# Kernel optimization log

Measured on AMD Instinct MI355X. Metric: run time of the kernel, lower is better.

## Reference

```python
import jax, jax.numpy as jnp
import numpy as np

N = 50000          # nodes
E = 800000         # edges (avg degree 16)
IN, HID, OUT = 128, 128, 32
BN_EPS = 1e-5


def gcn_conv(x, W, b, src, dst):
    """PyG GCNConv: D^-1/2 (A+I) D^-1/2 (x @ W) + b, self-loops included."""
    h = x @ W                                                  # [N, out]
    ones = jnp.ones((src.shape[0],), dtype=x.dtype)
    deg = jax.ops.segment_sum(ones, dst, num_segments=N) + 1.0  # in-degree + self-loop
    dis = jax.lax.rsqrt(deg)                                    # deg^-1/2
    norm = dis[src] * dis[dst]                                  # [E]
    msg = h[src] * norm[:, None]                                # gather + scale, [E, out]
    agg = jax.ops.segment_sum(msg, dst, num_segments=N)         # scatter-add
    agg = agg + h * (dis * dis)[:, None]                        # self-loop term (norm = 1/deg_i)
    return agg + b


def bn_relu(h, g, be):
    # BatchNorm1d in training mode: batch statistics over the node dimension
    mu = jnp.mean(h, axis=0)
    var = jnp.mean((h - mu) ** 2, axis=0)  # biased variance, as torch BN
    return jax.nn.relu((h - mu) * jax.lax.rsqrt(var + BN_EPS) * g + be)


def setup_inputs() -> dict:
    key = jax.random.key(0)
    ks = jax.random.split(key, 8)
    x = jax.random.normal(ks[0], (N, IN), dtype=jnp.float32)
    edge_index = jax.random.randint(ks[1], (2, E), 0, N, dtype=jnp.int64)
    W0 = jax.random.normal(ks[2], (IN, HID), dtype=jnp.float32) / np.sqrt(IN)
    W1 = jax.random.normal(ks[3], (HID, HID), dtype=jnp.float32) / np.sqrt(HID)
    W2 = jax.random.normal(ks[4], (HID, OUT), dtype=jnp.float32) / np.sqrt(HID)
    return {
        "x": x, "edge_index": edge_index,
        "W0": W0, "b0": jnp.zeros((HID,), jnp.float32),
        "g0": jnp.ones((HID,), jnp.float32), "be0": jnp.zeros((HID,), jnp.float32),
        "W1": W1, "b1": jnp.zeros((HID,), jnp.float32),
        "g1": jnp.ones((HID,), jnp.float32), "be1": jnp.zeros((HID,), jnp.float32),
        "W2": W2, "b2": jnp.zeros((OUT,), jnp.float32),
    }


def reference(x, edge_index, W0, b0, g0, be0, W1, b1, g1, be1, W2, b2):
    src, dst = edge_index[0], edge_index[1]
    # block 0: conv -> BN -> ReLU -> (dropout: eval, identity) -> residual
    h = bn_relu(gcn_conv(x, W0, b0, src, dst), g0, be0)
    x = h + x  # use_residual, in_channels == hidden, res_proj is None
    # block 1
    h = bn_relu(gcn_conv(x, W1, b1, src, dst), g1, be1)
    x = h + x
    # final conv + log_softmax over classes
    out = gcn_conv(x, W2, b2, src, dst)
    return jax.nn.log_softmax(out, axis=1)
```

## Files before the change

### kernel.cpp

```cpp
#include <hip/hip_runtime.h>
#include <math.h>

#define NN 50000
#define NNP (NN + 1)
#define NE 800000
#define NEP 1150000
#define NBLK 49
#define NBKT 7
#define BCAP 262144

typedef __attribute__((ext_vector_type(8))) short short8;
typedef __attribute__((ext_vector_type(4))) float float4v;

__device__ inline unsigned int f2bf(float f) {
  unsigned int u = __float_as_uint(f);
  return (u + 0x7fffu + ((u >> 16) & 1u)) >> 16;
}
__device__ inline unsigned int pack2bf(float lo, float hi) {
  return f2bf(lo) | (f2bf(hi) << 16);
}
__device__ inline float bflo(unsigned int p) { return __uint_as_float(p << 16); }
__device__ inline float bfhi(unsigned int p) { return __uint_as_float(p & 0xffff0000u); }

__device__ inline void bn_fold(const float* __restrict__ gstat, const float* __restrict__ g,
                               const float* __restrict__ be, float* __restrict__ bnabS, int tid) {
  if (tid < 128) {
    float s = 0.f, q = 0.f;
    #pragma unroll
    for (int r = 0; r < 8; r++) {
      s += gstat[r * 256 + tid];
      q += gstat[r * 256 + 128 + tid];
    }
    const float inv = 1.f / (float)NN;
    float m = s * inv;
    float var = q * inv - m * m;
    float a = rsqrtf(var + 1e-5f) * g[tid];
    bnabS[tid] = a;
    bnabS[128 + tid] = be[tid] - m * a;
  }
}


__global__ __launch_bounds__(256) void k_init(int* __restrict__ deg8, float* __restrict__ gstat,
                                              int* __restrict__ csr, int* __restrict__ binCnt,
                                              const float* __restrict__ W0, const float* __restrict__ W1,
                                              const float* __restrict__ W2,
                                              unsigned short* __restrict__ wt16) {
  int i = blockIdx.x * 256 + threadIdx.x;
  if (i < NEP) csr[i] = NN;
  if (i < 8 * NN) deg8[i] = 0;
  if (i < 4096) gstat[i] = 0.f;
  if (i < NBKT) binCnt[i] = 0;
  if (i < 32768) {
    int w = i >> 14;
    int rem = i & 16383;
    int k = rem >> 7;
    int n = rem & 127;
    const float* W = w ? W1 : W0;
    wt16[w * 16384 + n * 128 + k] = (unsigned short)f2bf(W[k * 128 + n]);
  } else if (i < 36864) {
    int idx = i - 32768;
    int n = idx >> 7;
    int k = idx & 127;
    wt16[32768 + n * 128 + k] = (unsigned short)f2bf(W2[k * 32 + n]);
  }
}


__global__ __launch_bounds__(1024) void k_binA(const int* __restrict__ src, const int* __restrict__ dst,
                                               int* __restrict__ deg8, int* __restrict__ binCnt,
                                               int2* __restrict__ bin) {
  __shared__ int lcnt[NBKT], lbase[NBKT];
  int tid = threadIdx.x;
  if (tid < NBKT) lcnt[tid] = 0;
  __syncthreads();
  int e = blockIdx.x * 1024 + tid;
  bool act = e < NE;
  int d = 0, s = 0, b = 0, rank = 0;
  if (act) {
    d = dst[e]; s = src[e];
    b = d >> 13;
    atomicAdd(&deg8[(e & 7) * NN + d], 1);
    rank = atomicAdd(&lcnt[b], 1);
  }
  __syncthreads();
  if (tid < NBKT && lcnt[tid] > 0) lbase[tid] = atomicAdd(&binCnt[tid], lcnt[tid]);
  __syncthreads();
  if (act) bin[(size_t)b * BCAP + lbase[b] + rank] = make_int2(d, s);
}

__global__ __launch_bounds__(1024) void k_scan1(const int* __restrict__ deg8, int* __restrict__ degtot,
                                                int* __restrict__ excl, int* __restrict__ blksum) {
  __shared__ int sm[1024];
  int t = threadIdx.x;
  int i = blockIdx.x * 1024 + t;
  int tot = 0;
  if (i < NN) {
    #pragma unroll
    for (int j = 0; j < 8; j++) tot += deg8[j * NN + i];
    degtot[i] = tot;
  }
  int v = (i < NN) ? ((tot + 7) & ~7) : 0;
  sm[t] = v;
  __syncthreads();
  for (int off = 1; off < 1024; off <<= 1) {
    int x = (t >= off) ? sm[t - off] : 0;
    __syncthreads();
    sm[t] += x;
    __syncthreads();
  }
  if (i < NN) excl[i] = sm[t] - v;
  if (t == 1023) blksum[blockIdx.x] = sm[t];
}

__global__ void k_scan2(const int* __restrict__ blksum, int* __restrict__ blkoff,
                        int* __restrict__ rowstart) {
  int t = threadIdx.x;
  int orig = (t < NBLK) ? blksum[t] : 0;
  int v = orig;
  #pragma unroll
  for (int off = 1; off < 64; off <<= 1) {
    int u = __shfl_up(v, off);
    if (t >= off) v += u;
  }
  if (t < NBLK) blkoff[t] = v - orig;
  if (t == NBLK - 1) rowstart[NN] = v;
}

__global__ __launch_bounds__(256) void k_scan3(int* __restrict__ excl, const int* __restrict__ blkoff,
                                               const int* __restrict__ degtot, int* __restrict__ cursor,
                                               float* __restrict__ dis,
                                               unsigned short* __restrict__ hs16, float* __restrict__ h2) {
  int i = blockIdx.x * 256 + threadIdx.x;
  if (i < NN) {
    int rs = excl[i] + blkoff[i >> 10];
    excl[i] = rs;
    cursor[i] = rs;
    dis[i] = rsqrtf((float)degtot[i] + 1.0f);
  }
  if (i < 64) {
    int slice = i >> 5, c = i & 31;
    ((unsigned int*)(hs16 + (size_t)slice * ((size_t)NNP * 64) + (size_t)NN * 64))[c] = 0u;
  }
  if (i < 32) h2[(size_t)NN * 32 + i] = 0.f;
}


__global__ __launch_bounds__(256) void k_fillB(const int2* __restrict__ bin, const int* __restrict__ binCnt,
                                               int* __restrict__ cursor, int* __restrict__ csr_src) {
  int b = blockIdx.x & 7;
  if (b >= NBKT) return;
  int q = blockIdx.x >> 3;
  int cnt = binCnt[b];
  const int2* __restrict__ B = bin + (size_t)b * BCAP;
  for (int i = q * 256 + threadIdx.x; i < cnt; i += 64 * 256) {
    int2 ds = B[i];
    int p = atomicAdd(&cursor[ds.x], 1);
    csr_src[p] = ds.y;
  }
}


__global__ __launch_bounds__(256) void k_gemm128(const float* __restrict__ X,
                                                 const unsigned short* __restrict__ Wt,
                                                 const float* __restrict__ dis,
                                                 unsigned short* __restrict__ hs16, int M) {
  __shared__ char smem[52224];
  unsigned short* A  = (unsigned short*)smem;
  unsigned short* Bt = (unsigned short*)(smem + 17408);
  float* C = (float*)smem;
  const int tid = threadIdx.x;
  const int row0 = blockIdx.x * 64;

  {
    int c4 = tid & 31;
    #pragma unroll
    for (int i = 0; i < 8; i++) {
      int r = (tid >> 5) + i * 8;
      int gr = row0 + r;
      float4 v = make_float4(0.f, 0.f, 0.f, 0.f);
      if (gr < M) v = *(const float4*)(X + (size_t)gr * 128 + c4 * 4);
      *(uint2*)(A + r * 136 + c4 * 4) = make_uint2(pack2bf(v.x, v.y), pack2bf(v.z, v.w));
    }
  }
  {
    int r = tid >> 1, h = (tid & 1) * 64;
    const uint4* src = (const uint4*)(Wt + r * 128 + h);
    uint4* dst = (uint4*)(Bt + r * 136 + h);
    #pragma unroll
    for (int i = 0; i < 8; i++) dst[i] = src[i];
  }
  __syncthreads();

  const int wv = tid >> 6;
  const int l = tid & 63;
  const int lm = l & 15;
  const int lq = l >> 4;

  float4v acc[8];
  #pragma unroll
  for (int j = 0; j < 8; j++) acc[j] = (float4v)(0.f);

  const unsigned short* Arow = A + (wv * 16 + lm) * 136 + lq * 8;
  #pragma unroll
  for (int ks = 0; ks < 4; ks++) {
    short8 af = *(const short8*)(Arow + ks * 32);
    #pragma unroll
    for (int j = 0; j < 8; j++) {
      short8 bf = *(const short8*)(Bt + (j * 16 + lm) * 136 + lq * 8 + ks * 32);
      acc[j] = __builtin_amdgcn_mfma_f32_16x16x32_bf16(af, bf, acc[j], 0, 0, 0);
    }
  }
  __syncthreads();

  #pragma unroll
  for (int j = 0; j < 8; j++) {
    int col = j * 16 + lm;
    int rbase = wv * 16 + lq * 4;
    #pragma unroll
    for (int r = 0; r < 4; r++) C[(rbase + r) * 132 + col] = acc[j][r];
  }
  __syncthreads();

  {
    #pragma unroll
    for (int i = 0; i < 4; i++) {
      int idx = tid + i * 256;
      int slice = idx >> 9;
      int r = (idx >> 3) & 63;
      int ch = idx & 7;
      int gr = row0 + r;
      if (gr < M) {
        float d = dis[gr];
        const float* cp = C + r * 132 + slice * 64 + ch * 8;
        uint4 u;
        u.x = pack2bf(cp[0] * d, cp[1] * d);
        u.y = pack2bf(cp[2] * d, cp[3] * d);
        u.z = pack2bf(cp[4] * d, cp[5] * d);
        u.w = pack2bf(cp[6] * d, cp[7] * d);
        *(uint4*)(hs16 + (size_t)slice * ((size_t)NNP * 64) + (size_t)gr * 64 + ch * 8) = u;
      }
    }
  }
}


__global__ __launch_bounds__(256) void k_gemm128f(const unsigned short* __restrict__ O16,
                                                  const float* __restrict__ Xin,
                                                  unsigned short* __restrict__ XA16,
                                                  const float* __restrict__ gstat,
                                                  const float* __restrict__ g,
                                                  const float* __restrict__ be,
                                                  const unsigned short* __restrict__ Wt,
                                                  const float* __restrict__ dis,
                                                  unsigned short* __restrict__ hs16, int M) {
  __shared__ char smem[52224];
  __shared__ float bnabS[256];
  unsigned short* A  = (unsigned short*)smem;
  unsigned short* Bt = (unsigned short*)(smem + 17408);
  float* C = (float*)smem;
  const int tid = threadIdx.x;
  const int row0 = blockIdx.x * 64;

  bn_fold(gstat, g, be, bnabS, tid);
  __syncthreads();

  {
    int c = tid & 15;
    float4 alo = *(const float4*)(bnabS + c * 8);
    float4 ahi = *(const float4*)(bnabS + c * 8 + 4);
    float4 clo = *(const float4*)(bnabS + 128 + c * 8);
    float4 chi = *(const float4*)(bnabS + 128 + c * 8 + 4);
    #pragma unroll
    for (int i = 0; i < 4; i++) {
      int r = (tid >> 4) + i * 16;
      int gr = row0 + r;
      uint4 u = make_uint4(0u, 0u, 0u, 0u);
      if (gr < M) {
        uint4 ou = *(const uint4*)(O16 + (size_t)gr * 128 + c * 8);
        float4 xlo = *(const float4*)(Xin + (size_t)gr * 128 + c * 8);
        float4 xhi = *(const float4*)(Xin + (size_t)gr * 128 + c * 8 + 4);
        float v0 = fmaxf(bflo(ou.x) * alo.x + clo.x, 0.f) + xlo.x;
        float v1 = fmaxf(bfhi(ou.x) * alo.y + clo.y, 0.f) + xlo.y;
        float v2 = fmaxf(bflo(ou.y) * alo.z + clo.z, 0.f) + xlo.z;
        float v3 = fmaxf(bfhi(ou.y) * alo.w + clo.w, 0.f) + xlo.w;
        float v4 = fmaxf(bflo(ou.z) * ahi.x + chi.x, 0.f) + xhi.x;
        float v5 = fmaxf(bfhi(ou.z) * ahi.y + chi.y, 0.f) + xhi.y;
        float v6 = fmaxf(bflo(ou.w) * ahi.z + chi.z, 0.f) + xhi.z;
        float v7 = fmaxf(bfhi(ou.w) * ahi.w + chi.w, 0.f) + xhi.w;
        u.x = pack2bf(v0, v1);
        u.y = pack2bf(v2, v3);
        u.z = pack2bf(v4, v5);
        u.w = pack2bf(v6, v7);
        *(uint4*)(XA16 + (size_t)gr * 128 + c * 8) = u;
      }
      *(uint4*)(A + r * 136 + c * 8) = u;
    }
  }
  {
    int r = tid >> 1, h = (tid & 1) * 64;
    const uint4* src = (const uint4*)(Wt + r * 128 + h);
    uint4* dst = (uint4*)(Bt + r * 136 + h);
    #pragma unroll
    for (int i = 0; i < 8; i++) dst[i] = src[i];
  }
  __syncthreads();

  const int wv = tid >> 6;
  const int l = tid & 63;
  const int lm = l & 15;
  const int lq = l >> 4;

  float4v acc[8];
  #pragma unroll
  for (int j = 0; j < 8; j++) acc[j] = (float4v)(0.f);

  const unsigned short* Arow = A + (wv * 16 + lm) * 136 + lq * 8;
  #pragma unroll
  for (int ks = 0; ks < 4; ks++) {
    short8 af = *(const short8*)(Arow + ks * 32);
    #pragma unroll
    for (int j = 0; j < 8; j++) {
      short8 bf = *(const short8*)(Bt + (j * 16 + lm) * 136 + lq * 8 + ks * 32);
      acc[j] = __builtin_amdgcn_mfma_f32_16x16x32_bf16(af, bf, acc[j], 0, 0, 0);
    }
  }
  __syncthreads();

  #pragma unroll
  for (int j = 0; j < 8; j++) {
    int col = j * 16 + lm;
    int rbase = wv * 16 + lq * 4;
    #pragma unroll
    for (int r = 0; r < 4; r++) C[(rbase + r) * 132 + col] = acc[j][r];
  }
  __syncthreads();

  {
    #pragma unroll
    for (int i = 0; i < 4; i++) {
      int idx = tid + i * 256;
      int slice = idx >> 9;
      int r = (idx >> 3) & 63;
      int ch = idx & 7;
      int gr = row0 + r;
      if (gr < M) {
        float d = dis[gr];
        const float* cp = C + r * 132 + slice * 64 + ch * 8;
        uint4 u;
        u.x = pack2bf(cp[0] * d, cp[1] * d);
        u.y = pack2bf(cp[2] * d, cp[3] * d);
        u.z = pack2bf(cp[4] * d, cp[5] * d);
        u.w = pack2bf(cp[6] * d, cp[7] * d);
        *(uint4*)(hs16 + (size_t)slice * ((size_t)NNP * 64) + (size_t)gr * 64 + ch * 8) = u;
      }
    }
  }
}


__global__ __launch_bounds__(256) void k_gemm32mf(const unsigned short* __restrict__ O16,
                                                  const unsigned short* __restrict__ XA16,
                                                  const float* __restrict__ gstat,
                                                  const float* __restrict__ g,
                                                  const float* __restrict__ be,
                                                  const unsigned short* __restrict__ Wt2,
                                                  const float* __restrict__ dis,
                                                  float* __restrict__ H, int M) {
  __shared__ char smem[26112];
  __shared__ float bnabS[256];
  unsigned short* A   = (unsigned short*)smem;
  unsigned short* Bt2 = (unsigned short*)(smem + 17408);
  float* C = (float*)smem;
  const int tid = threadIdx.x;
  const int row0 = blockIdx.x * 64;

  bn_fold(gstat, g, be, bnabS, tid);
  __syncthreads();

  {
    int c = tid & 15;
    float4 alo = *(const float4*)(bnabS + c * 8);
    float4 ahi = *(const float4*)(bnabS + c * 8 + 4);
    float4 clo = *(const float4*)(bnabS + 128 + c * 8);
    float4 chi = *(const float4*)(bnabS + 128 + c * 8 + 4);
    #pragma unroll
    for (int i = 0; i < 4; i++) {
      int r = (tid >> 4) + i * 16;
      int gr = row0 + r;
      uint4 u = make_uint4(0u, 0u, 0u, 0u);
      if (gr < M) {
        uint4 ou = *(const uint4*)(O16 + (size_t)gr * 128 + c * 8);
        uint4 xu = *(const uint4*)(XA16 + (size_t)gr * 128 + c * 8);
        float v0 = fmaxf(bflo(ou.x) * alo.x + clo.x, 0.f) + bflo(xu.x);
        float v1 = fmaxf(bfhi(ou.x) * alo.y + clo.y, 0.f) + bfhi(xu.x);
        float v2 = fmaxf(bflo(ou.y) * alo.z + clo.z, 0.f) + bflo(xu.y);
        float v3 = fmaxf(bfhi(ou.y) * alo.w + clo.w, 0.f) + bfhi(xu.y);
        float v4 = fmaxf(bflo(ou.z) * ahi.x + chi.x, 0.f) + bflo(xu.z);
        float v5 = fmaxf(bfhi(ou.z) * ahi.y + chi.y, 0.f) + bfhi(xu.z);
        float v6 = fmaxf(bflo(ou.w) * ahi.z + chi.z, 0.f) + bflo(xu.w);
        float v7 = fmaxf(bfhi(ou.w) * ahi.w + chi.w, 0.f) + bfhi(xu.w);
        u.x = pack2bf(v0, v1);
        u.y = pack2bf(v2, v3);
        u.z = pack2bf(v4, v5);
        u.w = pack2bf(v6, v7);
      }
      *(uint4*)(A + r * 136 + c * 8) = u;
    }
  }
  {
    int r = tid >> 3, h = (tid & 7) * 16;
    const uint4* src = (const uint4*)(Wt2 + r * 128 + h);
    uint4* dst = (uint4*)(Bt2 + r * 136 + h);
    dst[0] = src[0];
    dst[1] = src[1];
  }
  __syncthreads();

  const int wv = tid >> 6;
  const int l = tid & 63;
  const int lm = l & 15;
  const int lq = l >> 4;

  float4v acc[2];
  acc[0] = (float4v)(0.f);
  acc[1] = (float4v)(0.f);

  const unsigned short* Arow = A + (wv * 16 + lm) * 136 + lq * 8;
  #pragma unroll
  for (int ks = 0; ks < 4; ks++) {
    short8 af = *(const short8*)(Arow + ks * 32);
    #pragma unroll
    for (int j = 0; j < 2; j++) {
      short8 bf = *(const short8*)(Bt2 + (j * 16 + lm) * 136 + lq * 8 + ks * 32);
      acc[j] = __builtin_amdgcn_mfma_f32_16x16x32_bf16(af, bf, acc[j], 0, 0, 0);
    }
  }
  __syncthreads();

  #pragma unroll
  for (int j = 0; j < 2; j++) {
    int col = j * 16 + lm;
    int rbase = wv * 16 + lq * 4;
    #pragma unroll
    for (int r = 0; r < 4; r++) C[(rbase + r) * 36 + col] = acc[j][r];
  }
  __syncthreads();

  {
    #pragma unroll
    for (int i = 0; i < 2; i++) {
      int idx = tid + i * 256;
      int r = idx >> 3;
      int ch = idx & 7;
      int gr = row0 + r;
      if (gr < M) {
        float d = dis[gr];
        const float* cp = C + r * 36 + ch * 4;
        float4 v = make_float4(cp[0] * d, cp[1] * d, cp[2] * d, cp[3] * d);
        *(float4*)(H + (size_t)gr * 32 + ch * 4) = v;
      }
    }
  }
}


__global__ __launch_bounds__(256) void k_agg128s(const unsigned short* __restrict__ Hs,
                                                 const float* __restrict__ dis,
                                                 const int* __restrict__ rowstart,
                                                 const int* __restrict__ csr_src,
                                                 const float* __restrict__ bias,
                                                 unsigned short* __restrict__ out16,
                                                 float* __restrict__ gstat) {
  __shared__ float smS[4][128], smQ[4][128];
  const int tid = threadIdx.x;
  const int wv = tid >> 6;
  const int lane = tid & 63;
  const int node_sub = lane >> 3;
  const int fl = lane & 7;
  const int base = node_sub * 8;
  const int w = blockIdx.x * 32 + wv * 8 + node_sub;
  const bool act = w < NN;
  const unsigned short* __restrict__ S0 = Hs + fl * 8;
  const unsigned short* __restrict__ S1 = Hs + (size_t)NNP * 64 + fl * 8;
  float di = act ? dis[w] : 0.f;
  int e0 = 0, e1 = 0;
  if (act) { e0 = rowstart[w]; e1 = rowstart[w + 1]; }

  float a0[8], a1[8];
  #pragma unroll
  for (int j = 0; j < 8; j++) { a0[j] = 0.f; a1[j] = 0.f; }

  int idxCur = (e0 < e1) ? csr_src[e0 + fl] : 0;
  for (int e = e0; e < e1; e += 8) {
    int cur = idxCur;
    if (e + 8 < e1) idxCur = csr_src[e + 8 + fl];
    int s0 = __shfl(cur, base + 0), s1 = __shfl(cur, base + 1);
    int s2 = __shfl(cur, base + 2), s3 = __shfl(cur, base + 3);
    int s4 = __shfl(cur, base + 4), s5 = __shfl(cur, base + 5);
    int s6 = __shfl(cur, base + 6), s7 = __shfl(cur, base + 7);
    uint4 g0 = *(const uint4*)(S0 + (size_t)s0 * 64);
    uint4 g1 = *(const uint4*)(S0 + (size_t)s1 * 64);
    uint4 g2 = *(const uint4*)(S0 + (size_t)s2 * 64);
    uint4 g3 = *(const uint4*)(S0 + (size_t)s3 * 64);
    uint4 g4 = *(const uint4*)(S0 + (size_t)s4 * 64);
    uint4 g5 = *(const uint4*)(S0 + (size_t)s5 * 64);
    uint4 g6 = *(const uint4*)(S0 + (size_t)s6 * 64);
    uint4 g7 = *(const uint4*)(S0 + (size_t)s7 * 64);
    uint4 h0 = *(const uint4*)(S1 + (size_t)s0 * 64);
    uint4 h1 = *(const uint4*)(S1 + (size_t)s1 * 64);
    uint4 h2 = *(const uint4*)(S1 + (size_t)s2 * 64);
    uint4 h3 = *(const uint4*)(S1 + (size_t)s3 * 64);
    uint4 h4 = *(const uint4*)(S1 + (size_t)s4 * 64);
    uint4 h5 = *(const uint4*)(S1 + (size_t)s5 * 64);
    uint4 h6 = *(const uint4*)(S1 + (size_t)s6 * 64);
    uint4 h7 = *(const uint4*)(S1 + (size_t)s7 * 64);
    a0[0] += ((bflo(g0.x) + bflo(g1.x)) + (bflo(g2.x) + bflo(g3.x))) + ((bflo(g4.x) + bflo(g5.x)) + (bflo(g6.x) + bflo(g7.x)));
    a0[1] += ((bfhi(g0.x) + bfhi(g1.x)) + (bfhi(g2.x) + bfhi(g3.x))) + ((bfhi(g4.x) + bfhi(g5.x)) + (bfhi(g6.x) + bfhi(g7.x)));
    a0[2] += ((bflo(g0.y) + bflo(g1.y)) + (bflo(g2.y) + bflo(g3.y))) + ((bflo(g4.y) + bflo(g5.y)) + (bflo(g6.y) + bflo(g7.y)));
    a0[3] += ((bfhi(g0.y) + bfhi(g1.y)) + (bfhi(g2.y) + bfhi(g3.y))) + ((bfhi(g4.y) + bfhi(g5.y)) + (bfhi(g6.y) + bfhi(g7.y)));
    a0[4] += ((bflo(g0.z) + bflo(g1.z)) + (bflo(g2.z) + bflo(g3.z))) + ((bflo(g4.z) + bflo(g5.z)) + (bflo(g6.z) + bflo(g7.z)));
    a0[5] += ((bfhi(g0.z) + bfhi(g1.z)) + (bfhi(g2.z) + bfhi(g3.z))) + ((bfhi(g4.z) + bfhi(g5.z)) + (bfhi(g6.z) + bfhi(g7.z)));
    a0[6] += ((bflo(g0.w) + bflo(g1.w)) + (bflo(g2.w) + bflo(g3.w))) + ((bflo(g4.w) + bflo(g5.w)) + (bflo(g6.w) + bflo(g7.w)));
    a0[7] += ((bfhi(g0.w) + bfhi(g1.w)) + (bfhi(g2.w) + bfhi(g3.w))) + ((bfhi(g4.w) + bfhi(g5.w)) + (bfhi(g6.w) + bfhi(g7.w)));
    a1[0] += ((bflo(h0.x) + bflo(h1.x)) + (bflo(h2.x) + bflo(h3.x))) + ((bflo(h4.x) + bflo(h5.x)) + (bflo(h6.x) + bflo(h7.x)));
    a1[1] += ((bfhi(h0.x) + bfhi(h1.x)) + (bfhi(h2.x) + bfhi(h3.x))) + ((bfhi(h4.x) + bfhi(h5.x)) + (bfhi(h6.x) + bfhi(h7.x)));
    a1[2] += ((bflo(h0.y) + bflo(h1.y)) + (bflo(h2.y) + bflo(h3.y))) + ((bflo(h4.y) + bflo(h5.y)) + (bflo(h6.y) + bflo(h7.y)));
    a1[3] += ((bfhi(h0.y) + bfhi(h1.y)) + (bfhi(h2.y) + bfhi(h3.y))) + ((bfhi(h4.y) + bfhi(h5.y)) + (bfhi(h6.y) + bfhi(h7.y)));
    a1[4] += ((bflo(h0.z) + bflo(h1.z)) + (bflo(h2.z) + bflo(h3.z))) + ((bflo(h4.z) + bflo(h5.z)) + (bflo(h6.z) + bflo(h7.z)));
    a1[5] += ((bfhi(h0.z) + bfhi(h1.z)) + (bfhi(h2.z) + bfhi(h3.z))) + ((bfhi(h4.z) + bfhi(h5.z)) + (bfhi(h6.z) + bfhi(h7.z)));
    a1[6] += ((bflo(h0.w) + bflo(h1.w)) + (bflo(h2.w) + bflo(h3.w))) + ((bflo(h4.w) + bflo(h5.w)) + (bflo(h6.w) + bflo(h7.w)));
    a1[7] += ((bfhi(h0.w) + bfhi(h1.w)) + (bfhi(h2.w) + bfhi(h3.w))) + ((bfhi(h4.w) + bfhi(h5.w)) + (bfhi(h6.w) + bfhi(h7.w)));
  }

  float rv0[8], rv1[8];
  if (act) {
    uint4 sv0 = *(const uint4*)(S0 + (size_t)w * 64);
    uint4 sv1 = *(const uint4*)(S1 + (size_t)w * 64);
    float se0[8] = { bflo(sv0.x), bfhi(sv0.x), bflo(sv0.y), bfhi(sv0.y),
                     bflo(sv0.z), bfhi(sv0.z), bflo(sv0.w), bfhi(sv0.w) };
    float se1[8] = { bflo(sv1.x), bfhi(sv1.x), bflo(sv1.y), bfhi(sv1.y),
                     bflo(sv1.z), bfhi(sv1.z), bflo(sv1.w), bfhi(sv1.w) };
    #pragma unroll
    for (int j = 0; j < 8; j++) {
      rv0[j] = (a0[j] + se0[j]) * di + bias[fl * 8 + j];
      rv1[j] = (a1[j] + se1[j]) * di + bias[64 + fl * 8 + j];
    }
    uint4 u0, u1;
    u0.x = pack2bf(rv0[0], rv0[1]); u0.y = pack2bf(rv0[2], rv0[3]);
    u0.z = pack2bf(rv0[4], rv0[5]); u0.w = pack2bf(rv0[6], rv0[7]);
    u1.x = pack2bf(rv1[0], rv1[1]); u1.y = pack2bf(rv1[2], rv1[3]);
    u1.z = pack2bf(rv1[4], rv1[5]); u1.w = pack2bf(rv1[6], rv1[7]);
    *(uint4*)(out16 + (size_t)w * 128 + fl * 8)      = u0;
    *(uint4*)(out16 + (size_t)w * 128 + 64 + fl * 8) = u1;
  } else {
    #pragma unroll
    for (int j = 0; j < 8; j++) { rv0[j] = 0.f; rv1[j] = 0.f; }
  }

  float q0[8], q1[8];
  #pragma unroll
  for (int j = 0; j < 8; j++) { q0[j] = rv0[j] * rv0[j]; q1[j] = rv1[j] * rv1[j]; }
  #pragma unroll
  for (int off = 8; off <= 32; off <<= 1) {
    #pragma unroll
    for (int j = 0; j < 8; j++) {
      rv0[j] += __shfl_xor(rv0[j], off);
      q0[j]  += __shfl_xor(q0[j], off);
      rv1[j] += __shfl_xor(rv1[j], off);
      q1[j]  += __shfl_xor(q1[j], off);
    }
  }
  if (node_sub == 0) {
    #pragma unroll
    for (int j = 0; j < 8; j++) {
      smS[wv][fl * 8 + j] = rv0[j];      smQ[wv][fl * 8 + j] = q0[j];
      smS[wv][64 + fl * 8 + j] = rv1[j]; smQ[wv][64 + fl * 8 + j] = q1[j];
    }
  }
  __syncthreads();
  if (tid < 128) {
    float s = (smS[0][tid] + smS[1][tid]) + (smS[2][tid] + smS[3][tid]);
    float q = (smQ[0][tid] + smQ[1][tid]) + (smQ[2][tid] + smQ[3][tid]);
    int rep = blockIdx.x & 7;
    atomicAdd(&gstat[rep * 256 + tid], s);
    atomicAdd(&gstat[rep * 256 + 128 + tid], q);
  }
}


__global__ __launch_bounds__(256) void k_agg32lsm(const float* __restrict__ H2,
                                                  const float* __restrict__ dis,
                                                  const int* __restrict__ rowstart,
                                                  const int* __restrict__ csr_src,
                                                  const float* __restrict__ bias,
                                                  float* __restrict__ out) {
  int wave = (blockIdx.x * 256 + threadIdx.x) >> 6;
  int lane = threadIdx.x & 63;
  int half = lane >> 5;
  int l = lane & 31;
  int hbase = half * 32;
  int w = wave * 2 + half;
  if (w >= NN) return;
  const float* __restrict__ S = H2 + l;
  float di = dis[w];
  int e0 = rowstart[w], e1 = rowstart[w + 1];
  float acc = 0.f;
  for (int e = e0; e < e1; e += 8) {
    int myIdx = csr_src[e + (l & 7)];
    int s0 = __shfl(myIdx, hbase + 0), s1 = __shfl(myIdx, hbase + 1);
    int s2 = __shfl(myIdx, hbase + 2), s3 = __shfl(myIdx, hbase + 3);
    int s4 = __shfl(myIdx, hbase + 4), s5 = __shfl(myIdx, hbase + 5);
    int s6 = __shfl(myIdx, hbase + 6), s7 = __shfl(myIdx, hbase + 7);
    float h0 = S[(size_t)s0 * 32], h1 = S[(size_t)s1 * 32];
    float h2v = S[(size_t)s2 * 32], h3 = S[(size_t)s3 * 32];
    float h4 = S[(size_t)s4 * 32], h5 = S[(size_t)s5 * 32];
    float h6 = S[(size_t)s6 * 32], h7 = S[(size_t)s7 * 32];
    acc += ((h0 + h1) + (h2v + h3)) + ((h4 + h5) + (h6 + h7));
  }
  float v = (acc + S[(size_t)w * 32]) * di + bias[l];
  float m = v;
  #pragma unroll
  for (int off = 16; off >= 1; off >>= 1) m = fmaxf(m, __shfl_xor(m, off));
  float ex = expf(v - m);
  float s = ex;
  #pragma unroll
  for (int off = 16; off >= 1; off >>= 1) s += __shfl_xor(s, off);
  out[(size_t)w * 32 + l] = v - m - logf(s);
}


extern "C" void kernel_launch(void* const* d_in, const int* in_sizes, int n_in,
                              void* d_out, int out_size, void* d_ws, size_t ws_size,
                              hipStream_t stream) {
  const float* x   = (const float*)d_in[0];
  const int*   ei  = (const int*)d_in[1];
  const float* W0  = (const float*)d_in[2];
  const float* b0  = (const float*)d_in[3];
  const float* g0  = (const float*)d_in[4];
  const float* be0 = (const float*)d_in[5];
  const float* W1  = (const float*)d_in[6];
  const float* b1  = (const float*)d_in[7];
  const float* g1  = (const float*)d_in[8];
  const float* be1 = (const float*)d_in[9];
  const float* W2  = (const float*)d_in[10];
  const float* b2  = (const float*)d_in[11];
  float* out = (float*)d_out;
  const int* srcI = ei;
  const int* dstI = ei + NE;

  char* p = (char*)d_ws;
  auto take = [&](size_t bytes) { char* r = p; p += (bytes + 255) & ~(size_t)255; return (void*)r; };
  int*   deg8     = (int*)take((size_t)8 * NN * 4);
  int*   cursor   = (int*)take(NN * 4);
  int*   degtot   = (int*)take(NN * 4);
  int*   rowstart = (int*)take((NN + 1) * 4);
  int*   blksum   = (int*)take(64 * 4);
  int*   blkoff   = (int*)take(64 * 4);
  int*   binCnt   = (int*)take(8 * 4);
  float* dis      = (float*)take(NN * 4);
  int*   csr      = (int*)take((size_t)NEP * 4);
  int2*  bin      = (int2*)take((size_t)NBKT * BCAP * 8);
  float* gstat    = (float*)take(4096 * 4);
  unsigned short* wt16 = (unsigned short*)take((2 * 16384 + 4096) * 2);
  unsigned short* hs16 = (unsigned short*)take((size_t)NNP * 128 * 2);
  unsigned short* o16  = (unsigned short*)take((size_t)NN * 128 * 2);
  unsigned short* xA16 = (unsigned short*)take((size_t)NN * 128 * 2);
  float* h2       = (float*)take((size_t)NNP * 32 * 4);

  k_init<<<(NEP + 255) / 256, 256, 0, stream>>>(deg8, gstat, csr, binCnt, W0, W1, W2, wt16);
  k_binA<<<(NE + 1023) / 1024, 1024, 0, stream>>>(srcI, dstI, deg8, binCnt, bin);
  k_scan1<<<NBLK, 1024, 0, stream>>>(deg8, degtot, rowstart, blksum);
  k_scan2<<<1, 64, 0, stream>>>(blksum, blkoff, rowstart);
  k_scan3<<<(NN + 255) / 256, 256, 0, stream>>>(rowstart, blkoff, degtot, cursor, dis, hs16, h2);
  k_fillB<<<512, 256, 0, stream>>>(bin, binCnt, cursor, csr);

  const int aggGrid = (NN + 31) / 32;
  const int aggGrid32 = (NN + 7) / 8;

  k_gemm128<<<(NN + 63) / 64, 256, 0, stream>>>(x, wt16, dis, hs16, NN);
  k_agg128s<<<aggGrid, 256, 0, stream>>>(hs16, dis, rowstart, csr, b0, o16, gstat);

  k_gemm128f<<<(NN + 63) / 64, 256, 0, stream>>>(o16, x, xA16, gstat, g0, be0,
                                                 wt16 + 16384, dis, hs16, NN);
  k_agg128s<<<aggGrid, 256, 0, stream>>>(hs16, dis, rowstart, csr, b1, o16, gstat + 2048);

  k_gemm32mf<<<(NN + 63) / 64, 256, 0, stream>>>(o16, xA16, gstat + 2048, g1, be1,
                                                 wt16 + 32768, dis, h2, NN);
  k_agg32lsm<<<aggGrid32, 256, 0, stream>>>(h2, dis, rowstart, csr, b2, out);
}
```

Baseline: 290.0 us.

## Replace bucketed CSR build with direct atomic fill and fold scans together

Removes the dst-bucketing pass, which wrote (dst,src) pairs into per-bucket bins, and the pass that read those bins back. CSR is now filled directly from the edge list, with one atomic per edge on the cursor. The block scan now uses wavefront shuffles instead of a shared-memory Hillis-Steele loop, and the second-level scan is folded into k_scan3, which removes one launch. The trade is that fill atomics and csr writes become more scattered, since they are no longer grouped by dst range, which may hurt locality.

```diff
diff --git a/kernel.cpp b/kernel.cpp
--- a/kernel.cpp
+++ b/kernel.cpp
@@ -6,8 +6,6 @@
 #define NE 800000
 #define NEP 1150000
 #define NBLK 49
-#define NBKT 7
-#define BCAP 262144
 
 typedef __attribute__((ext_vector_type(8))) short short8;
 typedef __attribute__((ext_vector_type(4))) float float4v;
@@ -42,7 +40,7 @@
 
 
 __global__ __launch_bounds__(256) void k_init(int* __restrict__ deg8, float* __restrict__ gstat,
-                                              int* __restrict__ csr, int* __restrict__ binCnt,
+                                              int* __restrict__ csr,
                                               const float* __restrict__ W0, const float* __restrict__ W1,
                                               const float* __restrict__ W2,
                                               unsigned short* __restrict__ wt16) {
@@ -50,7 +48,6 @@
   if (i < NEP) csr[i] = NN;
   if (i < 8 * NN) deg8[i] = 0;
   if (i < 4096) gstat[i] = 0.f;
-  if (i < NBKT) binCnt[i] = 0;
   if (i < 32768) {
     int w = i >> 14;
     int rem = i & 16383;
@@ -67,33 +64,18 @@
 }
 
 
-__global__ __launch_bounds__(1024) void k_binA(const int* __restrict__ src, const int* __restrict__ dst,
-                                               int* __restrict__ deg8, int* __restrict__ binCnt,
-                                               int2* __restrict__ bin) {
-  __shared__ int lcnt[NBKT], lbase[NBKT];
-  int tid = threadIdx.x;
-  if (tid < NBKT) lcnt[tid] = 0;
-  __syncthreads();
-  int e = blockIdx.x * 1024 + tid;
-  bool act = e < NE;
-  int d = 0, s = 0, b = 0, rank = 0;
-  if (act) {
-    d = dst[e]; s = src[e];
-    b = d >> 13;
-    atomicAdd(&deg8[(e & 7) * NN + d], 1);
-    rank = atomicAdd(&lcnt[b], 1);
-  }
-  __syncthreads();
-  if (tid < NBKT && lcnt[tid] > 0) lbase[tid] = atomicAdd(&binCnt[tid], lcnt[tid]);
-  __syncthreads();
-  if (act) bin[(size_t)b * BCAP + lbase[b] + rank] = make_int2(d, s);
-}
+__global__ __launch_bounds__(256) void k_cnt(const int* __restrict__ dst, int* __restrict__ deg8) {
+  int e = blockIdx.x * 256 + threadIdx.x;
+  if (e < NE) atomicAdd(&deg8[(e & 7) * NN + dst[e]], 1);
+}
+
 
 __global__ __launch_bounds__(1024) void k_scan1(const int* __restrict__ deg8, int* __restrict__ degtot,
                                                 int* __restrict__ excl, int* __restrict__ blksum) {
-  __shared__ int sm[1024];
+  __shared__ int smW[16];
   int t = threadIdx.x;
   int i = blockIdx.x * 1024 + t;
+  int wv = t >> 6, ln = t & 63;
   int tot = 0;
   if (i < NN) {
     #pragma unroll
@@ -101,40 +83,58 @@
     degtot[i] = tot;
   }
   int v = (i < NN) ? ((tot + 7) & ~7) : 0;
-  sm[t] = v;
-  __syncthreads();
-  for (int off = 1; off < 1024; off <<= 1) {
-    int x = (t >= off) ? sm[t - off] : 0;
-    __syncthreads();
-    sm[t] += x;
-    __syncthreads();
-  }
-  if (i < NN) excl[i] = sm[t] - v;
-  if (t == 1023) blksum[blockIdx.x] = sm[t];
-}
-
-__global__ void k_scan2(const int* __restrict__ blksum, int* __restrict__ blkoff,
-                        int* __restrict__ rowstart) {
-  int t = threadIdx.x;
-  int orig = (t < NBLK) ? blksum[t] : 0;
-  int v = orig;
+  int sc = v;
   #pragma unroll
   for (int off = 1; off < 64; off <<= 1) {
-    int u = __shfl_up(v, off);
-    if (t >= off) v += u;
-  }
-  if (t < NBLK) blkoff[t] = v - orig;
-  if (t == NBLK - 1) rowstart[NN] = v;
-}
-
-__global__ __launch_bounds__(256) void k_scan3(int* __restrict__ excl, const int* __restrict__ blkoff,
+    int u = __shfl_up(sc, off);
+    if (ln >= off) sc += u;
+  }
+  if (ln == 63) smW[wv] = sc;
+  __syncthreads();
+  if (t < 64) {
+    int wsum = (t < 16) ? smW[t] : 0;
+    int s2 = wsum;
+    #pragma unroll
+    for (int off = 1; off < 16; off <<= 1) {
+      int u = __shfl_up(s2, off);
+      if (t >= off) s2 += u;
+    }
+    if (t < 16) smW[t] = s2 - wsum;
+    if (t == 15) blksum[blockIdx.x] = s2;
+  }
+  __syncthreads();
+  if (i < NN) excl[i] = (sc - v) + smW[wv];
+}
+
+
+__global__ __launch_bounds__(256) void k_scan3(int* __restrict__ rowstart, const int* __restrict__ blksum,
                                                const int* __restrict__ degtot, int* __restrict__ cursor,
                                                float* __restrict__ dis,
                                                unsigned short* __restrict__ hs16, float* __restrict__ h2) {
-  int i = blockIdx.x * 256 + threadIdx.x;
+  __shared__ int offS;
+  int tid = threadIdx.x;
+  int i = blockIdx.x * 256 + tid;
+  int myblk = blockIdx.x >> 2;
+  if (tid < 64) {
+    int bv = (tid < NBLK) ? blksum[tid] : 0;
+    int sc = bv;
+    #pragma unroll
+    for (int off = 1; off < 64; off <<= 1) {
+      int u = __shfl_up(sc, off);
+      if (tid >= off) sc += u;
+    }
+    int pre = (myblk > 0) ? __shfl(sc, myblk - 1) : 0;
+    int total = __shfl(sc, NBLK - 1);
+    if (tid == 0) {
+      offS = pre;
+      if (blockIdx.x == 0) rowstart[NN] = total;
+    }
+  }
+  __syncthreads();
+  int boff = offS;
   if (i < NN) {
-    int rs = excl[i] + blkoff[i >> 10];
-    excl[i] = rs;
+    int rs = rowstart[i] + boff;
+    rowstart[i] = rs;
     cursor[i] = rs;
     dis[i] = rsqrtf((float)degtot[i] + 1.0f);
   }
@@ -146,18 +146,13 @@
 }
 
 
-__global__ __launch_bounds__(256) void k_fillB(const int2* __restrict__ bin, const int* __restrict__ binCnt,
-                                               int* __restrict__ cursor, int* __restrict__ csr_src) {
-  int b = blockIdx.x & 7;
-  if (b >= NBKT) return;
-  int q = blockIdx.x >> 3;
-  int cnt = binCnt[b];
-  const int2* __restrict__ B = bin + (size_t)b * BCAP;
-  for (int i = q * 256 + threadIdx.x; i < cnt; i += 64 * 256) {
-    int2 ds = B[i];
-    int p = atomicAdd(&cursor[ds.x], 1);
-    csr_src[p] = ds.y;
-  }
+__global__ __launch_bounds__(256) void k_fill(const int* __restrict__ src, const int* __restrict__ dst,
+                                              int* __restrict__ cursor, int* __restrict__ csr_src) {
+  int e = blockIdx.x * 256 + threadIdx.x;
+  if (e >= NE) return;
+  int d = dst[e];
+  int p = atomicAdd(&cursor[d], 1);
+  csr_src[p] = src[e];
 }
 
 
@@ -656,11 +651,8 @@
   int*   degtot   = (int*)take(NN * 4);
   int*   rowstart = (int*)take((NN + 1) * 4);
   int*   blksum   = (int*)take(64 * 4);
-  int*   blkoff   = (int*)take(64 * 4);
-  int*   binCnt   = (int*)take(8 * 4);
   float* dis      = (float*)take(NN * 4);
   int*   csr      = (int*)take((size_t)NEP * 4);
-  int2*  bin      = (int2*)take((size_t)NBKT * BCAP * 8);
   float* gstat    = (float*)take(4096 * 4);
   unsigned short* wt16 = (unsigned short*)take((2 * 16384 + 4096) * 2);
   unsigned short* hs16 = (unsigned short*)take((size_t)NNP * 128 * 2);
@@ -668,12 +660,11 @@
   unsigned short* xA16 = (unsigned short*)take((size_t)NN * 128 * 2);
   float* h2       = (float*)take((size_t)NNP * 32 * 4);
 
-  k_init<<<(NEP + 255) / 256, 256, 0, stream>>>(deg8, gstat, csr, binCnt, W0, W1, W2, wt16);
-  k_binA<<<(NE + 1023) / 1024, 1024, 0, stream>>>(srcI, dstI, deg8, binCnt, bin);
+  k_init<<<(NEP + 255) / 256, 256, 0, stream>>>(deg8, gstat, csr, W0, W1, W2, wt16);
+  k_cnt<<<(NE + 255) / 256, 256, 0, stream>>>(dstI, deg8);
   k_scan1<<<NBLK, 1024, 0, stream>>>(deg8, degtot, rowstart, blksum);
-  k_scan2<<<1, 64, 0, stream>>>(blksum, blkoff, rowstart);
-  k_scan3<<<(NN + 255) / 256, 256, 0, stream>>>(rowstart, blkoff, degtot, cursor, dis, hs16, h2);
-  k_fillB<<<512, 256, 0, stream>>>(bin, binCnt, cursor, csr);
+  k_scan3<<<(NN + 255) / 256, 256, 0, stream>>>(rowstart, blksum, degtot, cursor, dis, hs16, h2);
+  k_fill<<<(NE + 255) / 256, 256, 0, stream>>>(srcI, dstI, cursor, csr);
 
   const int aggGrid = (NN + 31) / 32;
   const int aggGrid32 = (NN + 7) / 8;
```

New measurement: 303.5 us. 4.6% more time.
